# Kernel optimization log

Hardware: AMD Instinct MI355X
Metric: run time of the kernel (lower is better)

The kernel has to match this reference:

```python
import jax, jax.numpy as jnp
import numpy as np

NUM_FEATURES = 16
DIM = 32
NODES_PER_GRAPH = 64
BN_EPS = 1e-5


def _gin_layer(x, src, dst, Wa, ba, Wb, bb):
    # GINConv with eps=0: h = MLP(x + sum_{j in N(i)} x_j)
    agg = jax.ops.segment_sum(x[src], dst, num_segments=x.shape[0])
    h = x + agg
    h = jnp.maximum(h @ Wa + ba, 0.0) @ Wb + bb
    return h


def _bn(x, gamma, beta):
    m = x.mean(axis=0)
    v = x.var(axis=0)
    return gamma * (x - m) * jax.lax.rsqrt(v + BN_EPS) + beta


def setup_inputs() -> dict:
    key = jax.random.key(0)
    ks = jax.random.split(key, 16)
    batch = 8192
    n_nodes = batch * NODES_PER_GRAPH
    n_edges = 16 * n_nodes
    x = jax.random.normal(ks[0], (n_nodes, NUM_FEATURES), dtype=jnp.float32)
    edge_index = jax.random.randint(ks[1], (2, n_edges), 0, n_nodes, dtype=jnp.int32)
    s = 1.0 / np.sqrt(DIM)
    def lin(k, fin, fout):
        kw, kb = jax.random.split(k)
        lim = 1.0 / np.sqrt(fin)
        return (jax.random.uniform(kw, (fin, fout), jnp.float32, -lim, lim),
                jax.random.uniform(kb, (fout,), jnp.float32, -lim, lim))
    W1a, b1a = lin(ks[2], NUM_FEATURES, DIM)
    W1b, b1b = lin(ks[3], DIM, DIM)
    W2a, b2a = lin(ks[4], DIM, DIM)
    W2b, b2b = lin(ks[5], DIM, DIM)
    W3a, b3a = lin(ks[6], DIM, DIM)
    W3b, b3b = lin(ks[7], DIM, DIM)
    Wf, bf = lin(ks[8], DIM, 2)
    ones = jnp.ones((DIM,), jnp.float32)
    zeros = jnp.zeros((DIM,), jnp.float32)
    return {
        'x': x, 'edge_index': edge_index, 'batch': batch,
        'W1a': W1a, 'b1a': b1a, 'W1b': W1b, 'b1b': b1b,
        'W2a': W2a, 'b2a': b2a, 'W2b': W2b, 'b2b': b2b,
        'W3a': W3a, 'b3a': b3a, 'W3b': W3b, 'b3b': b3b,
        'g1': ones, 'be1': zeros, 'g2': ones, 'be2': zeros, 'g3': ones, 'be3': zeros,
        'Wf': Wf, 'bf': bf,
    }


def reference(x, edge_index, batch, W1a, b1a, W1b, b1b, W2a, b2a, W2b, b2b,
              W3a, b3a, W3b, b3b, g1, be1, g2, be2, g3, be3, Wf, bf):
    src, dst = edge_index[0], edge_index[1]
    h = x.reshape(-1, NUM_FEATURES)
    h = jnp.maximum(_gin_layer(h, src, dst, W1a, b1a, W1b, b1b), 0.0)
    h = _bn(h, g1, be1)
    h = jnp.maximum(_gin_layer(h, src, dst, W2a, b2a, W2b, b2b), 0.0)
    h = _bn(h, g2, be2)
    h = jnp.maximum(_gin_layer(h, src, dst, W3a, b3a, W3b, b3b), 0.0)
    h = _bn(h, g3, be3)
    h = h.reshape(batch, NODES_PER_GRAPH, DIM).sum(axis=1)  # sum-pool per graph
    # dropout p=0.3 is identity in eval mode
    logits = h @ Wf + bf
    return jax.nn.log_softmax(logits, axis=-1)
```

## Files before the change

kernel.cpp:

```cpp
#include <hip/hip_runtime.h>
#include <cstdint>
#include <cstddef>

#define NF 16
#define DIM 32
#define NCOARSE 512
#define SEGC 64
#define CCAP 18432

__device__ __forceinline__ float bf2f(unsigned short u) {
    return __uint_as_float(((unsigned int)u) << 16);
}
__device__ __forceinline__ unsigned short f2bf(float f) {
    unsigned int u = __float_as_uint(f);
    unsigned int r = (u + 0x7fffu + ((u >> 16) & 1u)) >> 16;
    return (unsigned short)r;
}

__global__ void __launch_bounds__(256) passA_k(const int* __restrict__ ei,
                                               int* __restrict__ counts,
                                               unsigned int* __restrict__ seg,
                                               int n_edges) {
    __shared__ int lcur[NCOARSE];
    int t = threadIdx.x;
    int blk = blockIdx.x;
    for (int i = t; i < NCOARSE; i += 256) lcur[i] = 0;
    __syncthreads();
    int base = blk * 16384;
    const int4* s4 = (const int4*)(ei + base);
    const int4* d4 = (const int4*)(ei + n_edges + base);
    size_t segbase = (size_t)blk * NCOARSE;
    for (int r = 0; r < 16; ++r) {
        int idx = r * 256 + t;
        int4 s = s4[idx];
        int4 d = d4[idx];
#define DOE(SS, DD)                                                           \
        {                                                                     \
            int c = ((unsigned int)(DD)) >> 10;                               \
            unsigned int val = ((unsigned int)(SS) << 10) |                   \
                               ((unsigned int)(DD) & 1023u);                  \
            int pos = atomicAdd(&lcur[c], 1);                                 \
            if (pos < SEGC) seg[(segbase + c) * SEGC + pos] = val;            \
        }
        DOE(s.x, d.x) DOE(s.y, d.y) DOE(s.z, d.z) DOE(s.w, d.w)
#undef DOE
    }
    __syncthreads();
    for (int i = t; i < NCOARSE; i += 256) counts[blk * NCOARSE + i] = min(lcur[i], SEGC);
}

__global__ void __launch_bounds__(256) passB_k(const unsigned int* __restrict__ seg,
                                               const int* __restrict__ counts,
                                               unsigned int* __restrict__ csr,
                                               int* __restrict__ rps, int* __restrict__ degs) {
    __shared__ int cnt[1024];
    __shared__ int cur[1024];
    __shared__ int sh[256];
    int t = threadIdx.x;
    int c = blockIdx.x;
    for (int i = t; i < 1024; i += 256) cnt[i] = 0;
    __syncthreads();
    for (int i = t; i < 512; i += 256) {
        int n = counts[i * NCOARSE + c];
        const unsigned int* sp = seg + ((size_t)i * NCOARSE + c) * SEGC;
        for (int k = 0; k < n; ++k) atomicAdd(&cnt[sp[k] & 1023u], 1);
    }
    __syncthreads();
    int c0 = cnt[4 * t], c1 = cnt[4 * t + 1], c2 = cnt[4 * t + 2], c3 = cnt[4 * t + 3];
    int lsum = c0 + c1 + c2 + c3;
    sh[t] = lsum;
    __syncthreads();
    for (int o = 1; o < 256; o <<= 1) {
        int v = 0;
        if (t >= o) v = sh[t - o];
        __syncthreads();
        if (t >= o) sh[t] += v;
        __syncthreads();
    }
    int excl = sh[t] - lsum;
    int base = c * CCAP + excl;
    cur[4 * t + 0] = base;
    cur[4 * t + 1] = base + c0;
    cur[4 * t + 2] = base + c0 + c1;
    cur[4 * t + 3] = base + c0 + c1 + c2;
    int node = c * 1024 + 4 * t;
    rps[node + 0] = base;
    rps[node + 1] = base + c0;
    rps[node + 2] = base + c0 + c1;
    rps[node + 3] = base + c0 + c1 + c2;
    degs[node + 0] = c0; degs[node + 1] = c1; degs[node + 2] = c2; degs[node + 3] = c3;
    __syncthreads();
    int limit = (c + 1) * CCAP;
    for (int i = t; i < 512; i += 256) {
        int n = counts[i * NCOARSE + c];
        const unsigned int* sp = seg + ((size_t)i * NCOARSE + c) * SEGC;
        for (int k = 0; k < n; ++k) {
            unsigned int v = sp[k];
            int pos = atomicAdd(&cur[v & 1023u], 1);
            if (pos < limit) csr[pos] = v >> 10;
        }
    }
}

__global__ void __launch_bounds__(256) xbf_k(const float* __restrict__ x,
                                             unsigned short* __restrict__ xb, int n8) {
    int t = blockIdx.x * 256 + threadIdx.x;
    if (t >= n8) return;
    const float4* p = (const float4*)x + 2 * (size_t)t;
    float4 a = p[0], b = p[1];
    uint4 o;
    o.x = (unsigned)f2bf(a.x) | ((unsigned)f2bf(a.y) << 16);
    o.y = (unsigned)f2bf(a.z) | ((unsigned)f2bf(a.w) << 16);
    o.z = (unsigned)f2bf(b.x) | ((unsigned)f2bf(b.y) << 16);
    o.w = (unsigned)f2bf(b.z) | ((unsigned)f2bf(b.w) << 16);
    ((uint4*)xb)[t] = o;
}

__global__ void __launch_bounds__(256) fused1_k(const float* __restrict__ x,
        const unsigned short* __restrict__ xb,
        const int* __restrict__ rps, const int* __restrict__ degs,
        const unsigned int* __restrict__ csr, unsigned short* __restrict__ hout,
        float* __restrict__ partials,
        const float* __restrict__ Wa, const float* __restrict__ ba,
        const float* __restrict__ Wb, const float* __restrict__ bb, int n_nodes) {
    __shared__ float lWa[NF * DIM];
    __shared__ float lWb[DIM * DIM];
    __shared__ float lbias[64];
    __shared__ float red[256];
    int t = threadIdx.x;
    for (int idx = t; idx < NF * DIM; idx += 256) lWa[idx] = Wa[idx];
    for (int idx = t; idx < DIM * DIM; idx += 256) lWb[idx] = Wb[idx];
    if (t < 32) lbias[t] = ba[t];
    else if (t < 64) lbias[t] = bb[t - 32];
    __syncthreads();

    int tid = blockIdx.x * 256 + t;
    int i = tid >> 2;
    int l = t & 3;
    int lane = t & 63;
    int gb = lane & ~3;
    unsigned int msk = (unsigned int)n_nodes - 1u;
    int q = l * 4;

    int dg = degs[i];
    int k = rps[i];
    float4 sx = *(const float4*)(x + (size_t)i * NF + q);
    float4 acc = make_float4(0.f, 0.f, 0.f, 0.f);
    if (dg > 0) {
        unsigned int my0 = csr[k + min(l, dg - 1)];
        unsigned int my1 = csr[k + min(l + 4, dg - 1)];
        for (int b = 0; b < dg; b += 8) {
            int s0 = (int)(__shfl(my0, gb + 0, 64) & msk);
            int s1 = (int)(__shfl(my0, gb + 1, 64) & msk);
            int s2 = (int)(__shfl(my0, gb + 2, 64) & msk);
            int s3 = (int)(__shfl(my0, gb + 3, 64) & msk);
            int s4 = (int)(__shfl(my1, gb + 0, 64) & msk);
            int s5 = (int)(__shfl(my1, gb + 1, 64) & msk);
            int s6 = (int)(__shfl(my1, gb + 2, 64) & msk);
            int s7 = (int)(__shfl(my1, gb + 3, 64) & msk);
            ushort4 v0 = *(const ushort4*)(xb + (size_t)s0 * NF + q);
            ushort4 v1 = *(const ushort4*)(xb + (size_t)s1 * NF + q);
            ushort4 v2 = *(const ushort4*)(xb + (size_t)s2 * NF + q);
            ushort4 v3 = *(const ushort4*)(xb + (size_t)s3 * NF + q);
            ushort4 v4 = *(const ushort4*)(xb + (size_t)s4 * NF + q);
            ushort4 v5 = *(const ushort4*)(xb + (size_t)s5 * NF + q);
            ushort4 v6 = *(const ushort4*)(xb + (size_t)s6 * NF + q);
            ushort4 v7 = *(const ushort4*)(xb + (size_t)s7 * NF + q);
            int nb = b + 8;
            if (nb < dg) {
                my0 = csr[k + min(nb + l, dg - 1)];
                my1 = csr[k + min(nb + l + 4, dg - 1)];
            }
            int rem = dg - b;
            float w1 = (1 < rem) ? 1.f : 0.f;
            float w2 = (2 < rem) ? 1.f : 0.f;
            float w3 = (3 < rem) ? 1.f : 0.f;
            float w4 = (4 < rem) ? 1.f : 0.f;
            float w5 = (5 < rem) ? 1.f : 0.f;
            float w6 = (6 < rem) ? 1.f : 0.f;
            float w7 = (7 < rem) ? 1.f : 0.f;
            acc.x += bf2f(v0.x); acc.y += bf2f(v0.y);
            acc.z += bf2f(v0.z); acc.w += bf2f(v0.w);
            acc.x = fmaf(w1, bf2f(v1.x), acc.x); acc.y = fmaf(w1, bf2f(v1.y), acc.y);
            acc.z = fmaf(w1, bf2f(v1.z), acc.z); acc.w = fmaf(w1, bf2f(v1.w), acc.w);
            acc.x = fmaf(w2, bf2f(v2.x), acc.x); acc.y = fmaf(w2, bf2f(v2.y), acc.y);
            acc.z = fmaf(w2, bf2f(v2.z), acc.z); acc.w = fmaf(w2, bf2f(v2.w), acc.w);
            acc.x = fmaf(w3, bf2f(v3.x), acc.x); acc.y = fmaf(w3, bf2f(v3.y), acc.y);
            acc.z = fmaf(w3, bf2f(v3.z), acc.z); acc.w = fmaf(w3, bf2f(v3.w), acc.w);
            acc.x = fmaf(w4, bf2f(v4.x), acc.x); acc.y = fmaf(w4, bf2f(v4.y), acc.y);
            acc.z = fmaf(w4, bf2f(v4.z), acc.z); acc.w = fmaf(w4, bf2f(v4.w), acc.w);
            acc.x = fmaf(w5, bf2f(v5.x), acc.x); acc.y = fmaf(w5, bf2f(v5.y), acc.y);
            acc.z = fmaf(w5, bf2f(v5.z), acc.z); acc.w = fmaf(w5, bf2f(v5.w), acc.w);
            acc.x = fmaf(w6, bf2f(v6.x), acc.x); acc.y = fmaf(w6, bf2f(v6.y), acc.y);
            acc.z = fmaf(w6, bf2f(v6.z), acc.z); acc.w = fmaf(w6, bf2f(v6.w), acc.w);
            acc.x = fmaf(w7, bf2f(v7.x), acc.x); acc.y = fmaf(w7, bf2f(v7.y), acc.y);
            acc.z = fmaf(w7, bf2f(v7.z), acc.z); acc.w = fmaf(w7, bf2f(v7.w), acc.w);
        }
    }
    float u[4] = { sx.x + acc.x, sx.y + acc.y, sx.z + acc.z, sx.w + acc.w };

    float tt[8];
#pragma unroll
    for (int j = 0; j < 8; ++j) tt[j] = lbias[l * 8 + j];
#pragma unroll
    for (int kk = 0; kk < NF; ++kk) {
        float uk = __shfl(u[kk & 3], gb + (kk >> 2), 64);
        const float4* wr = (const float4*)(lWa + kk * DIM + l * 8);
        float4 w0 = wr[0], w1 = wr[1];
        tt[0] = fmaf(uk, w0.x, tt[0]); tt[1] = fmaf(uk, w0.y, tt[1]);
        tt[2] = fmaf(uk, w0.z, tt[2]); tt[3] = fmaf(uk, w0.w, tt[3]);
        tt[4] = fmaf(uk, w1.x, tt[4]); tt[5] = fmaf(uk, w1.y, tt[5]);
        tt[6] = fmaf(uk, w1.z, tt[6]); tt[7] = fmaf(uk, w1.w, tt[7]);
    }
#pragma unroll
    for (int j = 0; j < 8; ++j) tt[j] = fmaxf(tt[j], 0.f);

    float o[8];
#pragma unroll
    for (int j = 0; j < 8; ++j) o[j] = lbias[32 + l * 8 + j];
#pragma unroll
    for (int kk = 0; kk < DIM; ++kk) {
        float tk = __shfl(tt[kk & 7], gb + (kk >> 3), 64);
        const float4* wr = (const float4*)(lWb + kk * DIM + l * 8);
        float4 w0 = wr[0], w1 = wr[1];
        o[0] = fmaf(tk, w0.x, o[0]); o[1] = fmaf(tk, w0.y, o[1]);
        o[2] = fmaf(tk, w0.z, o[2]); o[3] = fmaf(tk, w0.w, o[3]);
        o[4] = fmaf(tk, w1.x, o[4]); o[5] = fmaf(tk, w1.y, o[5]);
        o[6] = fmaf(tk, w1.z, o[6]); o[7] = fmaf(tk, w1.w, o[7]);
    }
    unsigned short b0 = f2bf(fmaxf(o[0], 0.f)), b1 = f2bf(fmaxf(o[1], 0.f));
    unsigned short b2 = f2bf(fmaxf(o[2], 0.f)), b3 = f2bf(fmaxf(o[3], 0.f));
    unsigned short b4 = f2bf(fmaxf(o[4], 0.f)), b5 = f2bf(fmaxf(o[5], 0.f));
    unsigned short b6 = f2bf(fmaxf(o[6], 0.f)), b7 = f2bf(fmaxf(o[7], 0.f));
    uint4 ov;
    ov.x = (unsigned)b0 | ((unsigned)b1 << 16);
    ov.y = (unsigned)b2 | ((unsigned)b3 << 16);
    ov.z = (unsigned)b4 | ((unsigned)b5 << 16);
    ov.w = (unsigned)b6 | ((unsigned)b7 << 16);
    *(uint4*)(hout + (size_t)i * DIM + l * 8) = ov;

    float s[8], ss[8];
    s[0]=bf2f(b0); s[1]=bf2f(b1); s[2]=bf2f(b2); s[3]=bf2f(b3);
    s[4]=bf2f(b4); s[5]=bf2f(b5); s[6]=bf2f(b6); s[7]=bf2f(b7);
#pragma unroll
    for (int j = 0; j < 8; ++j) ss[j] = s[j] * s[j];
#pragma unroll
    for (int m = 4; m <= 32; m <<= 1) {
#pragma unroll
        for (int j = 0; j < 8; ++j) {
            s[j] += __shfl_xor(s[j], m, 64);
            ss[j] += __shfl_xor(ss[j], m, 64);
        }
    }
    if (lane < 4) {
        int w = t >> 6;
#pragma unroll
        for (int j = 0; j < 8; ++j) {
            red[w * 64 + lane * 8 + j] = s[j];
            red[w * 64 + 32 + lane * 8 + j] = ss[j];
        }
    }
    __syncthreads();
    if (t < 64) {
        partials[(size_t)blockIdx.x * 64 + t] =
            red[t] + red[64 + t] + red[128 + t] + red[192 + t];
    }
}

__global__ void __launch_bounds__(256) fused23_k(const unsigned short* __restrict__ hin,
        const int* __restrict__ rps, const int* __restrict__ degs,
        const unsigned int* __restrict__ csr, unsigned short* __restrict__ hout,
        float* __restrict__ partials, const float* __restrict__ ab,
        const float* __restrict__ Wa, const float* __restrict__ ba,
        const float* __restrict__ Wb, const float* __restrict__ bb, int n_nodes) {
    __shared__ float lWa[DIM * DIM];
    __shared__ float lWb[DIM * DIM];
    __shared__ float lbias[64];
    __shared__ float lab[64];
    __shared__ float red[256];
    int t = threadIdx.x;
    for (int idx = t; idx < DIM * DIM; idx += 256) lWa[idx] = Wa[idx];
    for (int idx = t; idx < DIM * DIM; idx += 256) lWb[idx] = Wb[idx];
    if (t < 32) lbias[t] = ba[t];
    else if (t < 64) lbias[t] = bb[t - 32];
    if (t >= 64 && t < 128) lab[t - 64] = ab[t - 64];
    __syncthreads();

    int tid = blockIdx.x * 256 + t;
    int i = tid >> 3;
    int l = t & 7;
    int lane = t & 63;
    int gb = lane & ~7;
    unsigned int msk = (unsigned int)n_nodes - 1u;
    int q = l * 4;

    int dg = degs[i];
    int k = rps[i];
    ushort4 hv = *(const ushort4*)(hin + (size_t)i * DIM + q);
    float4 acc = make_float4(0.f, 0.f, 0.f, 0.f);
    if (dg > 0) {
        unsigned int my = csr[k + min(l, dg - 1)];
        for (int b = 0; b < dg; b += 8) {
            int s0 = (int)(__shfl(my, gb + 0, 64) & msk);
            int s1 = (int)(__shfl(my, gb + 1, 64) & msk);
            int s2 = (int)(__shfl(my, gb + 2, 64) & msk);
            int s3 = (int)(__shfl(my, gb + 3, 64) & msk);
            int s4 = (int)(__shfl(my, gb + 4, 64) & msk);
            int s5 = (int)(__shfl(my, gb + 5, 64) & msk);
            int s6 = (int)(__shfl(my, gb + 6, 64) & msk);
            int s7 = (int)(__shfl(my, gb + 7, 64) & msk);
            ushort4 v0 = *(const ushort4*)(hin + (size_t)s0 * DIM + q);
            ushort4 v1 = *(const ushort4*)(hin + (size_t)s1 * DIM + q);
            ushort4 v2 = *(const ushort4*)(hin + (size_t)s2 * DIM + q);
            ushort4 v3 = *(const ushort4*)(hin + (size_t)s3 * DIM + q);
            ushort4 v4 = *(const ushort4*)(hin + (size_t)s4 * DIM + q);
            ushort4 v5 = *(const ushort4*)(hin + (size_t)s5 * DIM + q);
            ushort4 v6 = *(const ushort4*)(hin + (size_t)s6 * DIM + q);
            ushort4 v7 = *(const ushort4*)(hin + (size_t)s7 * DIM + q);
            int nb = b + 8;
            if (nb < dg) my = csr[k + min(nb + l, dg - 1)];
            int rem = dg - b;
            float w1 = (1 < rem) ? 1.f : 0.f;
            float w2 = (2 < rem) ? 1.f : 0.f;
            float w3 = (3 < rem) ? 1.f : 0.f;
            float w4 = (4 < rem) ? 1.f : 0.f;
            float w5 = (5 < rem) ? 1.f : 0.f;
            float w6 = (6 < rem) ? 1.f : 0.f;
            float w7 = (7 < rem) ? 1.f : 0.f;
            acc.x += bf2f(v0.x); acc.y += bf2f(v0.y);
            acc.z += bf2f(v0.z); acc.w += bf2f(v0.w);
            acc.x = fmaf(w1, bf2f(v1.x), acc.x); acc.y = fmaf(w1, bf2f(v1.y), acc.y);
            acc.z = fmaf(w1, bf2f(v1.z), acc.z); acc.w = fmaf(w1, bf2f(v1.w), acc.w);
            acc.x = fmaf(w2, bf2f(v2.x), acc.x); acc.y = fmaf(w2, bf2f(v2.y), acc.y);
            acc.z = fmaf(w2, bf2f(v2.z), acc.z); acc.w = fmaf(w2, bf2f(v2.w), acc.w);
            acc.x = fmaf(w3, bf2f(v3.x), acc.x); acc.y = fmaf(w3, bf2f(v3.y), acc.y);
            acc.z = fmaf(w3, bf2f(v3.z), acc.z); acc.w = fmaf(w3, bf2f(v3.w), acc.w);
            acc.x = fmaf(w4, bf2f(v4.x), acc.x); acc.y = fmaf(w4, bf2f(v4.y), acc.y);
            acc.z = fmaf(w4, bf2f(v4.z), acc.z); acc.w = fmaf(w4, bf2f(v4.w), acc.w);
            acc.x = fmaf(w5, bf2f(v5.x), acc.x); acc.y = fmaf(w5, bf2f(v5.y), acc.y);
            acc.z = fmaf(w5, bf2f(v5.z), acc.z); acc.w = fmaf(w5, bf2f(v5.w), acc.w);
            acc.x = fmaf(w6, bf2f(v6.x), acc.x); acc.y = fmaf(w6, bf2f(v6.y), acc.y);
            acc.z = fmaf(w6, bf2f(v6.z), acc.z); acc.w = fmaf(w6, bf2f(v6.w), acc.w);
            acc.x = fmaf(w7, bf2f(v7.x), acc.x); acc.y = fmaf(w7, bf2f(v7.y), acc.y);
            acc.z = fmaf(w7, bf2f(v7.z), acc.z); acc.w = fmaf(w7, bf2f(v7.w), acc.w);
        }
    }
    float degp1 = (float)(dg + 1);
    float u[4];
    u[0] = fmaf(lab[q + 0], bf2f(hv.x) + acc.x, degp1 * lab[32 + q + 0]);
    u[1] = fmaf(lab[q + 1], bf2f(hv.y) + acc.y, degp1 * lab[32 + q + 1]);
    u[2] = fmaf(lab[q + 2], bf2f(hv.z) + acc.z, degp1 * lab[32 + q + 2]);
    u[3] = fmaf(lab[q + 3], bf2f(hv.w) + acc.w, degp1 * lab[32 + q + 3]);

    float tt[4];
#pragma unroll
    for (int c = 0; c < 4; ++c) tt[c] = lbias[l * 4 + c];
#pragma unroll
    for (int kk = 0; kk < DIM; ++kk) {
        float uk = __shfl(u[kk & 3], gb + (kk >> 2), 64);
        const float4* wr = (const float4*)(lWa + kk * DIM + l * 4);
        float4 w = wr[0];
        tt[0] = fmaf(uk, w.x, tt[0]); tt[1] = fmaf(uk, w.y, tt[1]);
        tt[2] = fmaf(uk, w.z, tt[2]); tt[3] = fmaf(uk, w.w, tt[3]);
    }
#pragma unroll
    for (int c = 0; c < 4; ++c) tt[c] = fmaxf(tt[c], 0.f);

    float o[4];
#pragma unroll
    for (int c = 0; c < 4; ++c) o[c] = lbias[32 + l * 4 + c];
#pragma unroll
    for (int kk = 0; kk < DIM; ++kk) {
        float tk = __shfl(tt[kk & 3], gb + (kk >> 2), 64);
        const float4* wr = (const float4*)(lWb + kk * DIM + l * 4);
        float4 w = wr[0];
        o[0] = fmaf(tk, w.x, o[0]); o[1] = fmaf(tk, w.y, o[1]);
        o[2] = fmaf(tk, w.z, o[2]); o[3] = fmaf(tk, w.w, o[3]);
    }
    unsigned short b0 = f2bf(fmaxf(o[0], 0.f)), b1 = f2bf(fmaxf(o[1], 0.f));
    unsigned short b2 = f2bf(fmaxf(o[2], 0.f)), b3 = f2bf(fmaxf(o[3], 0.f));
    uint2 ov;
    ov.x = (unsigned)b0 | ((unsigned)b1 << 16);
    ov.y = (unsigned)b2 | ((unsigned)b3 << 16);
    *(uint2*)(hout + (size_t)i * DIM + l * 4) = ov;

    float s[4], ss[4];
    s[0] = bf2f(b0); s[1] = bf2f(b1); s[2] = bf2f(b2); s[3] = bf2f(b3);
#pragma unroll
    for (int c = 0; c < 4; ++c) ss[c] = s[c] * s[c];
#pragma unroll
    for (int m = 8; m <= 32; m <<= 1) {
#pragma unroll
        for (int c = 0; c < 4; ++c) {
            s[c] += __shfl_xor(s[c], m, 64);
            ss[c] += __shfl_xor(ss[c], m, 64);
        }
    }
    if (lane < 8) {
        int w = t >> 6;
#pragma unroll
        for (int c = 0; c < 4; ++c) {
            red[w * 64 + lane * 4 + c] = s[c];
            red[w * 64 + 32 + lane * 4 + c] = ss[c];
        }
    }
    __syncthreads();
    if (t < 64) {
        partials[(size_t)blockIdx.x * 64 + t] =
            red[t] + red[64 + t] + red[128 + t] + red[192 + t];
    }
}

__global__ void __launch_bounds__(256) red_k(const float* __restrict__ partials,
                                             float* __restrict__ sums, int rows) {
    __shared__ float sd[256];
    int t = threadIdx.x;
    int col = t & 63;
    int rpb = rows >> 7;
    int r0 = blockIdx.x * rpb + (t >> 6);
    int rend = blockIdx.x * rpb + rpb;
    float s = 0.f;
    for (int r = r0; r < rend; r += 4) s += partials[(size_t)r * 64 + col];
    sd[t] = s;
    __syncthreads();
    if (t < 64) {
        float tot = sd[t] + sd[t + 64] + sd[t + 128] + sd[t + 192];
        unsafeAtomicAdd(&sums[t], tot);
    }
}

__global__ void bn_fin_k(const float* __restrict__ sums, const float* __restrict__ gamma,
                         const float* __restrict__ beta, float* __restrict__ ab,
                         float inv_n) {
    int c = threadIdx.x;
    if (c >= DIM) return;
    float mean = sums[c] * inv_n;
    float var = sums[DIM + c] * inv_n - mean * mean;
    float a = gamma[c] * rsqrtf(var + 1e-5f);
    ab[c] = a;
    ab[DIM + c] = beta[c] - a * mean;
}

__global__ void pool_head_k(const unsigned short* __restrict__ h, const float* __restrict__ ab3,
                            const float* __restrict__ Wf, const float* __restrict__ bf,
                            float* __restrict__ out, int n_graphs) {
    int g = blockIdx.x;
    if (g >= n_graphs) return;
    int lane = threadIdx.x;
    int c = lane & 31;
    int half = lane >> 5;
    const unsigned short* base = h + ((size_t)g * 64 + (size_t)half * 32) * DIM;
    float s = 0.0f;
#pragma unroll
    for (int n = 0; n < 32; ++n) s += bf2f(base[(size_t)n * DIM + c]);
    s += __shfl_xor(s, 32);
    float a = ab3[c], b = ab3[DIM + c];
    s = fmaf(a, s, 64.0f * b);
    float p0 = s * Wf[c * 2 + 0];
    float p1 = s * Wf[c * 2 + 1];
#pragma unroll
    for (int o = 16; o > 0; o >>= 1) {
        p0 += __shfl_xor(p0, o);
        p1 += __shfl_xor(p1, o);
    }
    if (lane == 0) {
        float z0 = p0 + bf[0];
        float z1 = p1 + bf[1];
        float m = fmaxf(z0, z1);
        float lse = m + logf(expf(z0 - m) + expf(z1 - m));
        out[(size_t)g * 2 + 0] = z0 - lse;
        out[(size_t)g * 2 + 1] = z1 - lse;
    }
}

extern "C" void kernel_launch(void* const* d_in, const int* in_sizes, int n_in,
                              void* d_out, int out_size, void* d_ws, size_t ws_size,
                              hipStream_t stream) {
    const float* x  = (const float*)d_in[0];
    const int*   ei = (const int*)d_in[1];
    const float* W1a = (const float*)d_in[3];
    const float* b1a = (const float*)d_in[4];
    const float* W1b = (const float*)d_in[5];
    const float* b1b = (const float*)d_in[6];
    const float* W2a = (const float*)d_in[7];
    const float* b2a = (const float*)d_in[8];
    const float* W2b = (const float*)d_in[9];
    const float* b2b = (const float*)d_in[10];
    const float* W3a = (const float*)d_in[11];
    const float* b3a = (const float*)d_in[12];
    const float* W3b = (const float*)d_in[13];
    const float* b3b = (const float*)d_in[14];
    const float* g1  = (const float*)d_in[15];
    const float* be1 = (const float*)d_in[16];
    const float* g2  = (const float*)d_in[17];
    const float* be2 = (const float*)d_in[18];
    const float* g3  = (const float*)d_in[19];
    const float* be3 = (const float*)d_in[20];
    const float* Wf  = (const float*)d_in[21];
    const float* bf  = (const float*)d_in[22];
    float* out = (float*)d_out;

    int n_nodes  = in_sizes[0] / NF;
    int n_edges  = in_sizes[1] / 2;
    int n_graphs = n_nodes / 64;
    float inv_n = 1.0f / (float)n_nodes;

    char* ws = (char*)d_ws;
    size_t off = 0;
    unsigned int* seg = (unsigned int*)(ws + off);
    float* partials = (float*)(ws + off);
    unsigned short* Hb = (unsigned short*)(ws + off + (size_t)8 * 1024 * 1024);
    unsigned short* xb = (unsigned short*)(ws + off + (size_t)40 * 1024 * 1024);
    off += (size_t)n_nodes * DIM * sizeof(float);
    unsigned short* Ha = (unsigned short*)(ws + off); off += (size_t)n_nodes * DIM * sizeof(short);
    unsigned int* csr = (unsigned int*)(ws + off); off += (size_t)NCOARSE * CCAP * sizeof(int);
    int* rps    = (int*)(ws + off);  off += (size_t)n_nodes * sizeof(int);
    int* degs   = (int*)(ws + off);  off += (size_t)n_nodes * sizeof(int);
    int* counts = (int*)(ws + off);  off += (size_t)512 * NCOARSE * sizeof(int);
    float* stats = (float*)(ws + off);
    float* sums1 = stats;        float* ab1 = stats + 64;
    float* sums2 = stats + 128;  float* ab2 = stats + 192;
    float* sums3 = stats + 256;  float* ab3 = stats + 320;

    const int BT = 256;
    int f1_blocks = n_nodes / 64;
    int f23_blocks = n_nodes / 32;
    int xb_threads = n_nodes * NF / 8;

    hipMemsetAsync(stats, 0, 384 * sizeof(float), stream);

    passA_k<<<512, BT, 0, stream>>>(ei, counts, seg, n_edges);
    passB_k<<<NCOARSE, BT, 0, stream>>>(seg, counts, csr, rps, degs);

    xbf_k<<<(xb_threads + BT - 1) / BT, BT, 0, stream>>>(x, xb, xb_threads);

    fused1_k<<<f1_blocks, BT, 0, stream>>>(x, xb, rps, degs, csr, Ha, partials,
                                           W1a, b1a, W1b, b1b, n_nodes);
    red_k<<<128, BT, 0, stream>>>(partials, sums1, f1_blocks);
    bn_fin_k<<<1, 64, 0, stream>>>(sums1, g1, be1, ab1, inv_n);

    fused23_k<<<f23_blocks, BT, 0, stream>>>(Ha, rps, degs, csr, Hb, partials, ab1,
                                             W2a, b2a, W2b, b2b, n_nodes);
    red_k<<<128, BT, 0, stream>>>(partials, sums2, f23_blocks);
    bn_fin_k<<<1, 64, 0, stream>>>(sums2, g2, be2, ab2, inv_n);

    fused23_k<<<f23_blocks, BT, 0, stream>>>(Hb, rps, degs, csr, Ha, partials, ab2,
                                             W3a, b3a, W3b, b3b, n_nodes);
    red_k<<<128, BT, 0, stream>>>(partials, sums3, f23_blocks);
    bn_fin_k<<<1, 64, 0, stream>>>(sums3, g3, be3, ab3, inv_n);

    pool_head_k<<<n_graphs, 64, 0, stream>>>(Ha, ab3, Wf, bf, out, n_graphs);
}
```

Before: 871.3 us.

## Stage edge bucketing and CSR scatter in LDS, then write coalesced

Both CSR-building passes now scatter into shared memory instead of global memory. Pass A fills a padded per-coarse-bucket LDS buffer and then copies it out one wavefront-row at a time. Pass B builds each coarse block's CSR slice in a dynamic LDS array and writes it out contiguously. This replaces scattered global stores with coalesced ones, at the cost of large LDS allocations (about 133KB and 74KB) that limit occupancy to roughly one block per CU.

Result: faster. 720.5 us, median of 2 (-17.3%).

```diff
diff --git a/kernel.cpp b/kernel.cpp
--- a/kernel.cpp
+++ b/kernel.cpp
@@ -6,6 +6,7 @@
 #define DIM 32
 #define NCOARSE 512
 #define SEGC 64
+#define SEGP 65
 #define CCAP 18432
 
 __device__ __forceinline__ float bf2f(unsigned short u) {
@@ -21,7 +22,9 @@
                                                int* __restrict__ counts,
                                                unsigned int* __restrict__ seg,
                                                int n_edges) {
-    __shared__ int lcur[NCOARSE];
+    extern __shared__ unsigned int dynA[];
+    unsigned int* lseg = dynA;
+    int* lcur = (int*)(dynA + NCOARSE * SEGP);
     int t = threadIdx.x;
     int blk = blockIdx.x;
     for (int i = t; i < NCOARSE; i += 256) lcur[i] = 0;
@@ -29,7 +32,6 @@
     int base = blk * 16384;
     const int4* s4 = (const int4*)(ei + base);
     const int4* d4 = (const int4*)(ei + n_edges + base);
-    size_t segbase = (size_t)blk * NCOARSE;
     for (int r = 0; r < 16; ++r) {
         int idx = r * 256 + t;
         int4 s = s4[idx];
@@ -40,12 +42,18 @@
             unsigned int val = ((unsigned int)(SS) << 10) |                   \
                                ((unsigned int)(DD) & 1023u);                  \
             int pos = atomicAdd(&lcur[c], 1);                                 \
-            if (pos < SEGC) seg[(segbase + c) * SEGC + pos] = val;            \
+            if (pos < SEGC) lseg[c * SEGP + pos] = val;                       \
         }
         DOE(s.x, d.x) DOE(s.y, d.y) DOE(s.z, d.z) DOE(s.w, d.w)
 #undef DOE
     }
     __syncthreads();
+    int lane = t & 63;
+    int w = t >> 6;
+    size_t segbase = (size_t)blk * NCOARSE * SEGC;
+    for (int c = w; c < NCOARSE; c += 4) {
+        seg[segbase + (size_t)c * SEGC + lane] = lseg[c * SEGP + lane];
+    }
     for (int i = t; i < NCOARSE; i += 256) counts[blk * NCOARSE + i] = min(lcur[i], SEGC);
 }
 
@@ -56,6 +64,7 @@
     __shared__ int cnt[1024];
     __shared__ int cur[1024];
     __shared__ int sh[256];
+    extern __shared__ unsigned int lcsr[];
     int t = threadIdx.x;
     int c = blockIdx.x;
     for (int i = t; i < 1024; i += 256) cnt[i] = 0;
@@ -78,28 +87,30 @@
         __syncthreads();
     }
     int excl = sh[t] - lsum;
-    int base = c * CCAP + excl;
-    cur[4 * t + 0] = base;
-    cur[4 * t + 1] = base + c0;
-    cur[4 * t + 2] = base + c0 + c1;
-    cur[4 * t + 3] = base + c0 + c1 + c2;
+    cur[4 * t + 0] = excl;
+    cur[4 * t + 1] = excl + c0;
+    cur[4 * t + 2] = excl + c0 + c1;
+    cur[4 * t + 3] = excl + c0 + c1 + c2;
+    int gbase = c * CCAP + excl;
     int node = c * 1024 + 4 * t;
-    rps[node + 0] = base;
-    rps[node + 1] = base + c0;
-    rps[node + 2] = base + c0 + c1;
-    rps[node + 3] = base + c0 + c1 + c2;
+    rps[node + 0] = gbase;
+    rps[node + 1] = gbase + c0;
+    rps[node + 2] = gbase + c0 + c1;
+    rps[node + 3] = gbase + c0 + c1 + c2;
     degs[node + 0] = c0; degs[node + 1] = c1; degs[node + 2] = c2; degs[node + 3] = c3;
     __syncthreads();
-    int limit = (c + 1) * CCAP;
     for (int i = t; i < 512; i += 256) {
         int n = counts[i * NCOARSE + c];
         const unsigned int* sp = seg + ((size_t)i * NCOARSE + c) * SEGC;
         for (int k = 0; k < n; ++k) {
             unsigned int v = sp[k];
             int pos = atomicAdd(&cur[v & 1023u], 1);
-            if (pos < limit) csr[pos] = v >> 10;
-        }
-    }
+            if (pos < CCAP) lcsr[pos] = v >> 10;
+        }
+    }
+    __syncthreads();
+    size_t cbase = (size_t)c * CCAP;
+    for (int idx = t; idx < CCAP; idx += 256) csr[cbase + idx] = lcsr[idx];
 }
 
 __global__ void __launch_bounds__(256) xbf_k(const float* __restrict__ x,
@@ -527,10 +538,13 @@
     int f23_blocks = n_nodes / 32;
     int xb_threads = n_nodes * NF / 8;
 
+    size_t passA_lds = ((size_t)NCOARSE * SEGP + NCOARSE) * sizeof(int);
+    size_t passB_lds = (size_t)CCAP * sizeof(int);
+
     hipMemsetAsync(stats, 0, 384 * sizeof(float), stream);
 
-    passA_k<<<512, BT, 0, stream>>>(ei, counts, seg, n_edges);
-    passB_k<<<NCOARSE, BT, 0, stream>>>(seg, counts, csr, rps, degs);
+    passA_k<<<512, BT, passA_lds, stream>>>(ei, counts, seg, n_edges);
+    passB_k<<<NCOARSE, BT, passB_lds, stream>>>(seg, counts, csr, rps, degs);
 
     xbf_k<<<(xb_threads + BT - 1) / BT, BT, 0, stream>>>(x, xb, xb_threads);
 
```
